# Performance work log

Hardware: AMD Instinct MI355X
Metric: run time of the kernel (lower is better)

The kernel has to match this reference:

```python
import jax, jax.numpy as jnp
import numpy as np

VOCAB, EMB = 30000, 300
HEADS, DPH = 8, 50
AD = HEADS * DPH            # att_dim_total = 400
MAX_LINES, MAX_WPL = 128, 32
BATCH = 16
NEG = 1e7                   # padding-mask penalty, matches torch source


def _split_heads(x):
    # [N, S, AD] -> [N, H, S, D]
    return x.reshape(x.shape[0], -1, HEADS, DPH).transpose(0, 2, 1, 3)


def _attention(q, k, v, mask_q=None, mask_k=None, mask_v=None):
    # Faithful port of MTHiSAN._attention. Note the (oddly named) torch masks:
    #   mask_q masks the KEY axis of scores, mask_k/mask_v zero the QUERY axis.
    scale = float(np.sqrt(q.shape[-1]))
    scores = jnp.einsum('bhqd,bhkd->bhqk', q, k) / scale
    if mask_q is not None:
        scores = scores - NEG * (~mask_q)[:, None, None, :].astype(scores.dtype)
    w = jax.nn.softmax(scores, axis=-1)
    if mask_k is not None:
        w = w * mask_k[:, None, :, None].astype(w.dtype)
    out = jnp.einsum('bhqk,bhkd->bhqd', w, v)
    if mask_v is not None:
        out = out * mask_v[:, None, :, None].astype(out.dtype)
    return out


def _forward(docs, emb, wq_w, wq_b, wk_w, wk_b, wv_w, wv_b, w_tgt,
             lq_w, lq_b, lk_w, lk_b, lv_w, lv_b, l_tgt,
             fc1_w, fc1_b, fc2_w, fc2_b):
    B = docs.shape[0]
    d = docs[:, :MAX_LINES * MAX_WPL].reshape(B * MAX_LINES, MAX_WPL)
    mask_w = d != 0                               # [B*L, W]
    mask_l = mask_w.sum(-1) != 0                  # [B*L]  non-empty lines
    # NOTE: instead of gathering non-empty lines (data-dependent shape), we keep
    # full shapes; masked word attention yields exact zeros for empty lines,
    # equivalent to the torch scatter into new_zeros.
    we = emb[d]                                   # [B*L, W, E] (dropout = eval/no-op)
    wq = jax.nn.elu(_split_heads(we @ wq_w + wq_b))
    wk = jax.nn.elu(_split_heads(we @ wk_w + wk_b))
    wv = jax.nn.elu(_split_heads(we @ wv_w + wv_b))
    watt = _attention(wq, wk, wv, mask_w, mask_w, mask_w)   # [B*L,H,W,D]
    # learned word-level target query (Linear(1, AD)(ones) == weight vector)
    tgt = jnp.broadcast_to(w_tgt.reshape(1, HEADS, 1, DPH),
                           (B * MAX_LINES, HEADS, 1, DPH))
    line_e = _attention(tgt, wk, watt, mask_q=mask_w)       # [B*L,H,1,D]
    line_e = line_e.transpose(0, 2, 1, 3).reshape(B * MAX_LINES, AD)
    line_e = line_e * mask_l[:, None].astype(line_e.dtype)  # zero empty lines
    line_e = line_e.reshape(B, MAX_LINES, AD)
    mask_l2 = mask_l.reshape(B, MAX_LINES)
    lq = jax.nn.elu(_split_heads(line_e @ lq_w + lq_b))
    lk = jax.nn.elu(_split_heads(line_e @ lk_w + lk_b))
    lv = jax.nn.elu(_split_heads(line_e @ lv_w + lv_b))
    latt = _attention(lq, lk, lv, mask_l2, mask_l2, mask_l2)  # [B,H,L,D]
    dtgt = jnp.broadcast_to(l_tgt.reshape(1, HEADS, 1, DPH), (B, HEADS, 1, DPH))
    doc_e = _attention(dtgt, lk, latt, mask_q=mask_l2)        # [B,H,1,D]
    doc_e = doc_e.transpose(0, 2, 1, 3).reshape(B, AD)
    logits1 = doc_e @ fc1_w + fc1_b   # task 'site'      [B,70]
    logits2 = doc_e @ fc2_w + fc2_b   # task 'histology' [B,512]
    return jnp.concatenate([logits1, logits2], axis=1)


def setup_inputs() -> dict:
    key = jax.random.key(0)
    ks = jax.random.split(key, 20)
    xavier = lambda k, i, o: (jax.random.normal(k, (i, o), jnp.float32)
                              * np.float32(np.sqrt(2.0 / (i + o))))
    emb = jax.random.normal(ks[0], (VOCAB, EMB), jnp.float32) * 0.02
    emb = emb.at[0].set(0.0)  # padding row zeroed as in __init__
    docs = jax.random.randint(ks[1], (BATCH, MAX_LINES * MAX_WPL), 0, VOCAB)
    z = lambda n: jnp.zeros((n,), jnp.float32)
    return dict(
        docs=docs, emb=emb,
        wq_w=xavier(ks[2], EMB, AD), wq_b=z(AD),
        wk_w=xavier(ks[3], EMB, AD), wk_b=z(AD),
        wv_w=xavier(ks[4], EMB, AD), wv_b=z(AD),
        w_tgt=jax.random.uniform(ks[5], (AD,), jnp.float32),
        lq_w=xavier(ks[6], AD, AD), lq_b=z(AD),
        lk_w=xavier(ks[7], AD, AD), lk_b=z(AD),
        lv_w=xavier(ks[8], AD, AD), lv_b=z(AD),
        l_tgt=jax.random.uniform(ks[9], (AD,), jnp.float32),
        fc1_w=xavier(ks[10], AD, 70), fc1_b=z(70),
        fc2_w=xavier(ks[11], AD, 512), fc2_b=z(512),
    )


def reference(docs, emb, wq_w, wq_b, wk_w, wk_b, wv_w, wv_b, w_tgt,
              lq_w, lq_b, lk_w, lk_b, lv_w, lv_b, l_tgt,
              fc1_w, fc1_b, fc2_w, fc2_b):
    return _forward(docs, emb, wq_w, wq_b, wk_w, wk_b, wv_w, wv_b, w_tgt,
                    lq_w, lq_b, lk_w, lk_b, lv_w, lv_b, l_tgt,
                    fc1_w, fc1_b, fc2_w, fc2_b)
```

## Files before the change

### kernel.cpp

```cpp
#include <hip/hip_runtime.h>
#include <math.h>

#define NLINES 2048
#define WPL 32
#define EMBD 300
#define AD 400
#define NH 8
#define DPH 50
#define QKV_S 52
#define SC_S 36
#define BATCH 16
#define LPD 128
#define NCOLS 1200
#define NPAD 1280
#define WLINE_FL 39936
#define HBLK 4992

typedef __bf16 bf16;
typedef bf16  v8bf  __attribute__((ext_vector_type(8)));
typedef float v4f   __attribute__((ext_vector_type(4)));
typedef float v16f  __attribute__((ext_vector_type(16)));

__device__ __forceinline__ float elu(float x) {
    return x > 0.f ? x : expm1f(x);
}
__device__ __forceinline__ float elu_fast(float x) {
    return x > 0.f ? x : (__expf(x) - 1.f);
}

#define SCALE 7.0710678118654755f

__global__ void split_rows_packed(const float* __restrict__ src,
                                  bf16* __restrict__ pk,
                                  int rows, int K, int K2)
{
    long idx = (long)blockIdx.x * 256 + threadIdx.x;
    if (idx >= (long)rows * K2) return;
    int r = (int)(idx / K2), k = (int)(idx - (long)r * K2);
    float x = (k < K) ? src[(long)r * K + k] : 0.f;
    bf16 h = (bf16)x;
    float hf = (float)h;
    bf16 l = (bf16)(x - hf);
    const long p = ((long)r * (K2 >> 3) + (k >> 3)) * 16 + (k & 7);
    pk[p] = h; pk[p + 8] = l;
}

__global__ void split_wt_packed(const float* __restrict__ W0, const float* __restrict__ W1,
                                const float* __restrict__ W2,
                                const float* __restrict__ B0, const float* __restrict__ B1,
                                const float* __restrict__ B2,
                                bf16* __restrict__ pk,
                                float* __restrict__ biasCat, int K, int K2)
{
    long idx = (long)blockIdx.x * 256 + threadIdx.x;
    if (idx >= (long)NPAD * K2) return;
    int n = (int)(idx / K2), k = (int)(idx - (long)n * K2);
    float x = 0.f;
    if (k < K && n < NCOLS) {
        int p = n / 400, c = n - p * 400;
        const float* W = (p == 0) ? W0 : (p == 1) ? W1 : W2;
        x = W[(long)k * 400 + c];
    }
    bf16 h = (bf16)x;
    float hf = (float)h;
    bf16 l = (bf16)(x - hf);
    const long pidx = ((long)(k >> 3) * NPAD + n) * 16 + (k & 7);
    pk[pidx] = h; pk[pidx + 8] = l;
    if (k == 0) {
        float b = 0.f;
        if (n < NCOLS) {
            int p = n / 400, c = n - p * 400;
            const float* Bp = (p == 0) ? B0 : (p == 1) ? B1 : B2;
            b = Bp[c];
        }
        biasCat[n] = b;
    }
}

__launch_bounds__(256, 4)
__global__ void mfma_gemm(const bf16* __restrict__ Ap,
                          const int* __restrict__ docs,
                          const bf16* __restrict__ Bp,
                          const float* __restrict__ biasCat,
                          float* __restrict__ C, int K2, int word_layout)
{
    __shared__ int tok[128];

    const int tid = threadIdx.x;

    const int total = (int)(gridDim.x * gridDim.y);
    int flat = (int)(blockIdx.y * gridDim.x + blockIdx.x);
    if ((total & 7) == 0) flat = (flat & 7) * (total >> 3) + (flat >> 3);
    const int bx = flat % (int)gridDim.x;
    const int by = flat / (int)gridDim.x;
    const int row0 = by * 128;
    const int n0 = bx * 128;

    if (tid < 128) tok[tid] = docs ? docs[row0 + tid] : (row0 + tid);
    __syncthreads();

    const int wv = tid >> 6, lane = tid & 63;
    const int half = lane >> 5, r32 = lane & 31;
    const int wm0 = (wv >> 1) * 64, wn0 = (wv & 1) * 64;

    const int colA = n0 + wn0 + r32;
    const int colB = colA + 32;

    const long a0 = (long)tok[wm0 + r32]      * ((long)K2 * 2);
    const long a1 = (long)tok[wm0 + 32 + r32] * ((long)K2 * 2);

    v16f acc[2][2];
    #pragma unroll
    for (int a = 0; a < 2; ++a)
        #pragma unroll
        for (int b = 0; b < 2; ++b) acc[a][b] = (v16f)0.f;

    const int nk = K2 >> 5;
    for (int kt = 0; kt < nk; ++kt) {
        #pragma unroll
        for (int ks = 0; ks < 2; ++ks) {
            const int k0 = kt * 32 + (ks * 2 + half) * 8;
            const bf16* bg = Bp + (long)(k0 >> 3) * NPAD * 16;
            const long ka = (long)k0 * 2;
            v8bf fb_h[2], fb_l[2], fa_h[2], fa_l[2];
            fb_h[0] = *(const v8bf*)&bg[(long)colA * 16];
            fb_l[0] = *(const v8bf*)&bg[(long)colA * 16 + 8];
            fb_h[1] = *(const v8bf*)&bg[(long)colB * 16];
            fb_l[1] = *(const v8bf*)&bg[(long)colB * 16 + 8];
            fa_h[0] = *(const v8bf*)&Ap[a0 + ka];
            fa_l[0] = *(const v8bf*)&Ap[a0 + ka + 8];
            fa_h[1] = *(const v8bf*)&Ap[a1 + ka];
            fa_l[1] = *(const v8bf*)&Ap[a1 + ka + 8];

            #pragma unroll
            for (int mt = 0; mt < 2; ++mt)
                #pragma unroll
                for (int nt = 0; nt < 2; ++nt)
                    acc[mt][nt] = __builtin_amdgcn_mfma_f32_32x32x16_bf16(fa_h[mt], fb_h[nt], acc[mt][nt], 0, 0, 0);
            #pragma unroll
            for (int mt = 0; mt < 2; ++mt)
                #pragma unroll
                for (int nt = 0; nt < 2; ++nt)
                    acc[mt][nt] = __builtin_amdgcn_mfma_f32_32x32x16_bf16(fa_h[mt], fb_l[nt], acc[mt][nt], 0, 0, 0);
            #pragma unroll
            for (int mt = 0; mt < 2; ++mt)
                #pragma unroll
                for (int nt = 0; nt < 2; ++nt)
                    acc[mt][nt] = __builtin_amdgcn_mfma_f32_32x32x16_bf16(fa_l[mt], fb_h[nt], acc[mt][nt], 0, 0, 0);
        }
    }

    if (word_layout) {
        #pragma unroll
        for (int nt = 0; nt < 2; ++nt) {
            const int col = n0 + wn0 + nt * 32 + r32;
            if (col >= NCOLS) continue;
            const float bv = biasCat[col];
            const int p = col / 400;
            const int rem = col - p * 400;
            const int hh = rem / 50;
            const int d  = rem - hh * 50;
            #pragma unroll
            for (int mt = 0; mt < 2; ++mt) {
                const int rbase = row0 + wm0 + mt * 32 + 4 * half;
                #pragma unroll
                for (int rg = 0; rg < 16; ++rg) {
                    const int row = rbase + (rg & 3) + 8 * (rg >> 2);
                    const int ln = row >> 5, r = row & 31;
                    const long base = (((long)ln * NH + hh) * 3 + p) * 1664 + r * 52;
                    const float x = acc[mt][nt][rg] + bv;
                    C[base + d] = elu_fast(x);
                    if (d == 49) {
                        float2 z; z.x = 0.f; z.y = 0.f;
                        *(float2*)&C[base + 50] = z;
                    }
                }
            }
        }
    } else {
        #pragma unroll
        for (int nt = 0; nt < 2; ++nt) {
            const int col = n0 + wn0 + nt * 32 + r32;
            if (col >= NCOLS) continue;
            const float bv = biasCat[col];
            #pragma unroll
            for (int mt = 0; mt < 2; ++mt) {
                const int rbase = row0 + wm0 + mt * 32 + 4 * half;
                #pragma unroll
                for (int rg = 0; rg < 16; ++rg) {
                    const int row = rbase + (rg & 3) + 8 * (rg >> 2);
                    const float x = acc[mt][nt][rg] + bv;
                    C[(long)row * NCOLS + col] = elu_fast(x);
                }
            }
        }
    }
}

__launch_bounds__(256)
__global__ void word_attn4(const float* __restrict__ qkvw, const int* __restrict__ docs,
                           const float* __restrict__ w_tgt,
                           float* __restrict__ line_e, float* __restrict__ mask_l)
{
    __shared__ __align__(16) float sh[HBLK];
    __shared__ float sc[32 * 33];
    __shared__ float msk[WPL];
    __shared__ float tw[WPL];
    __shared__ float coefA[WPL];
    __shared__ float part[8][33];
    __shared__ float cw[WPL];
    __shared__ float vpart[4][64];
    __shared__ float tg[52];
    __shared__ float mls_s;

    const int tid = threadIdx.x;
    const int line = blockIdx.x >> 3;
    const int h = blockIdx.x & 7;

    if (tid < WPL) msk[tid] = (docs[line * WPL + tid] != 0) ? 1.f : 0.f;
    if (tid >= 64 && tid < 116) tg[tid - 64] = (tid - 64 < DPH) ? w_tgt[h * DPH + tid - 64] : 0.f;

    const float* src = qkvw + ((long)line * NH + h) * HBLK;
    for (int i = tid; i < HBLK / 4; i += 256)
        *(float4*)&sh[i * 4] = *(const float4*)&src[i * 4];
    __syncthreads();

    if (tid == 0) {
        float m = 0.f;
        for (int w = 0; w < WPL; ++w) m = fmaxf(m, msk[w]);
        mls_s = m;
        if (h == 0) mask_l[line] = m;
    }

    const int j = tid >> 3, kg = tid & 7;
    float4 qv[13];
    #pragma unroll
    for (int i = 0; i < 13; ++i) qv[i] = *(const float4*)&sh[j * 52 + i * 4];

    float e4[4];
    float m = -1e30f;
    #pragma unroll
    for (int c = 0; c < 4; ++c) {
        const int kk = kg * 4 + c;
        const float* kr = &sh[1664 + kk * 52];
        float s = 0.f;
        #pragma unroll
        for (int i = 0; i < 13; ++i) {
            const float4 kv = *(const float4*)&kr[i * 4];
            s += qv[i].x * kv.x + qv[i].y * kv.y + qv[i].z * kv.z + qv[i].w * kv.w;
        }
        s = s / SCALE - 1e7f * (1.f - msk[kk]);
        e4[c] = s;
        m = fmaxf(m, s);
    }
    m = fmaxf(m, __shfl_xor(m, 1));
    m = fmaxf(m, __shfl_xor(m, 2));
    m = fmaxf(m, __shfl_xor(m, 4));
    float rsum = 0.f;
    #pragma unroll
    for (int c = 0; c < 4; ++c) { e4[c] = __expf(e4[c] - m); rsum += e4[c]; }
    rsum += __shfl_xor(rsum, 1);
    rsum += __shfl_xor(rsum, 2);
    rsum += __shfl_xor(rsum, 4);
    #pragma unroll
    for (int c = 0; c < 4; ++c) sc[j * 33 + kg * 4 + c] = e4[c];

    if (tid < WPL) {
        const float* kr = &sh[1664 + tid * 52];
        float s = 0.f;
        #pragma unroll
        for (int i = 0; i < 25; ++i)
            s += tg[2 * i] * kr[2 * i] + tg[2 * i + 1] * kr[2 * i + 1];
        s = s / SCALE - 1e7f * (1.f - msk[tid]);
        float tm = s;
        #pragma unroll
        for (int off = 16; off >= 1; off >>= 1) tm = fmaxf(tm, __shfl_xor(tm, off, 32));
        const float te = __expf(s - tm);
        float tsum = te;
        #pragma unroll
        for (int off = 16; off >= 1; off >>= 1) tsum += __shfl_xor(tsum, off, 32);
        tw[tid] = te / tsum;
    }
    __syncthreads();

    if (kg == 0) coefA[j] = tw[j] * msk[j] / rsum;
    __syncthreads();

    {
        const int k = tid & 31, jg = tid >> 5;
        float cv = 0.f;
        #pragma unroll
        for (int t = 0; t < 4; ++t) {
            const int jj = jg * 4 + t;
            cv += coefA[jj] * sc[jj * 33 + k];
        }
        part[jg][k] = cv;
    }
    __syncthreads();
    if (tid < WPL) {
        float cv = 0.f;
        #pragma unroll
        for (int g = 0; g < 8; ++g) cv += part[g][tid];
        cw[tid] = cv;
    }
    __syncthreads();

    {
        const int d = tid & 63, kh = tid >> 6;
        float acc = 0.f;
        if (d < 52) {
            #pragma unroll
            for (int t = 0; t < 8; ++t) {
                const int k = kh * 8 + t;
                acc += cw[k] * sh[3328 + k * 52 + d];
            }
        }
        vpart[kh][d] = acc;
    }
    __syncthreads();
    if (tid < DPH) {
        const float o = vpart[0][tid] + vpart[1][tid] + vpart[2][tid] + vpart[3][tid];
        line_e[(long)line * AD + h * DPH + tid] = o * mls_s;
    }
}

__launch_bounds__(256)
__global__ void line_attn2(const float* __restrict__ Q, const float* __restrict__ Kp,
                           const float* __restrict__ Vp,
                           long DS, long HS, long LS,
                           const float* __restrict__ l_tgt, const float* __restrict__ mask_l,
                           float* __restrict__ doc_e)
{
    __shared__ float kl[LPD * 52];
    __shared__ float sc[64 * 130];
    __shared__ float ml[LPD];
    __shared__ float tw[LPD];
    __shared__ float cw[LPD];
    __shared__ float coefA[64];
    __shared__ float pm[4 * 64];
    __shared__ float ps[4 * 64];
    __shared__ float tg[52];
    __shared__ float rr[2];
    __shared__ float vpart[2][64];

    const int tid = threadIdx.x;
    const int doc = blockIdx.x >> 3;
    const int h = blockIdx.x & 7;
    const float* qbase = Q + doc * DS + h * HS;
    const float* kbase = Kp + doc * DS + h * HS;
    const float* vbase = Vp + doc * DS + h * HS;

    if (tid < LPD) { ml[tid] = mask_l[doc * LPD + tid]; cw[tid] = 0.f; }
    if (tid < 52) tg[tid] = (tid < DPH) ? l_tgt[h * DPH + tid] : 0.f;
    for (int idx = tid; idx < LPD * 52; idx += 256) {
        const int r = idx / 52, d = idx - r * 52;
        kl[idx] = (d < DPH) ? kbase[(long)r * LS + d] : 0.f;
    }
    __syncthreads();

    if (tid < LPD) {
        const float* kr = &kl[tid * 52];
        float s = 0.f;
        #pragma unroll
        for (int i = 0; i < 25; ++i)
            s += tg[2 * i] * kr[2 * i] + tg[2 * i + 1] * kr[2 * i + 1];
        tw[tid] = s / SCALE - 1e7f * (1.f - ml[tid]);
    }
    __syncthreads();
    if (tid < 64) {
        float a = fmaxf(tw[tid], tw[64 + tid]);
        #pragma unroll
        for (int off = 32; off >= 1; off >>= 1) a = fmaxf(a, __shfl_xor(a, off));
        if (tid == 0) rr[0] = a;
    }
    __syncthreads();
    if (tid < 64) {
        const float tm2 = rr[0];
        float a = __expf(tw[tid] - tm2) + __expf(tw[64 + tid] - tm2);
        #pragma unroll
        for (int off = 32; off >= 1; off >>= 1) a += __shfl_xor(a, off);
        if (tid == 0) rr[1] = a;
    }
    __syncthreads();
    if (tid < LPD) tw[tid] = __expf(tw[tid] - rr[0]) / rr[1];
    __syncthreads();

    const int j2 = tid & 63;
    const int kq = tid >> 6;

    for (int g = 0; g < 2; ++g) {
        const int j = g * 64 + j2;
        float2 qv[25];
        #pragma unroll
        for (int i = 0; i < 25; ++i)
            qv[i] = *(const float2*)(qbase + (long)j * LS + 2 * i);

        float m = -1e30f;
        for (int c = 0; c < 32; ++c) {
            const int k = kq * 32 + c;
            const float* kr = &kl[k * 52];
            float s = 0.f;
            #pragma unroll
            for (int i = 0; i < 25; ++i)
                s += qv[i].x * kr[2 * i] + qv[i].y * kr[2 * i + 1];
            s = s / SCALE - 1e7f * (1.f - ml[k]);
            sc[j2 * 130 + k] = s;
            m = fmaxf(m, s);
        }
        pm[kq * 64 + j2] = m;
        __syncthreads();
        const float rowm = fmaxf(fmaxf(pm[j2], pm[64 + j2]),
                                 fmaxf(pm[128 + j2], pm[192 + j2]));
        float sum = 0.f;
        for (int c = 0; c < 32; ++c) {
            const int k = kq * 32 + c;
            const float e = __expf(sc[j2 * 130 + k] - rowm);
            sc[j2 * 130 + k] = e;
            sum += e;
        }
        ps[kq * 64 + j2] = sum;
        __syncthreads();
        if (kq == 0) {
            const float rs = ps[j2] + ps[64 + j2] + ps[128 + j2] + ps[192 + j2];
            coefA[j2] = tw[j] * ml[j] / rs;
        }
        __syncthreads();
        if (tid < LPD) {
            float cv = 0.f;
            for (int jj = 0; jj < 64; ++jj)
                cv += coefA[jj] * sc[jj * 130 + tid];
            cw[tid] += cv;
        }
        __syncthreads();
    }

    const int d = tid & 63;
    const int half = (tid >> 6) & 1;
    if (tid < 128 && d < DPH) {
        float acc = 0.f;
        for (int k = half * 64; k < half * 64 + 64; ++k)
            acc += cw[k] * vbase[(long)k * LS + d];
        vpart[half][d] = acc;
    }
    __syncthreads();
    if (tid < DPH)
        doc_e[doc * AD + h * DPH + tid] = vpart[0][tid] + vpart[1][tid];
}

__launch_bounds__(256)
__global__ void word_attn(const float* __restrict__ qkv, const int* __restrict__ docs,
                          const float* __restrict__ w_tgt,
                          float* __restrict__ line_e, float* __restrict__ mask_l)
{
    __shared__ float qs[WPL * QKV_S];
    __shared__ float ks[WPL * QKV_S];
    __shared__ float vs[WPL * QKV_S];
    __shared__ float sc[WPL * SC_S];
    __shared__ float ts[WPL], tw[WPL], cw[WPL], msk[WPL];
    __shared__ float mls;

    const int tid = threadIdx.x;
    const int line = blockIdx.x;

    if (tid < WPL) msk[tid] = (docs[line * WPL + tid] != 0) ? 1.f : 0.f;
    __syncthreads();
    if (tid == 0) {
        float ml = 0.f;
        for (int w = 0; w < WPL; ++w) ml = fmaxf(ml, msk[w]);
        mls = ml;
        mask_l[line] = ml;
    }
    for (int h = 0; h < NH; ++h) {
        for (int idx = tid; idx < WPL * DPH; idx += 256) {
            const int r = idx / DPH, d = idx - r * DPH;
            const size_t base = (size_t)(line * WPL + r) * NCOLS + h * DPH + d;
            qs[r * QKV_S + d] = qkv[base];
            ks[r * QKV_S + d] = qkv[base + 400];
            vs[r * QKV_S + d] = qkv[base + 800];
        }
        __syncthreads();
        {
            const int j = tid >> 3, kg = tid & 7;
            #pragma unroll
            for (int c = 0; c < 4; ++c) {
                const int kk = kg * 4 + c;
                float s = 0.f;
                for (int dd = 0; dd < DPH; ++dd)
                    s += qs[j * QKV_S + dd] * ks[kk * QKV_S + dd];
                sc[j * SC_S + kk] = s / SCALE - 1e7f * (1.f - msk[kk]);
            }
        }
        if (tid < WPL) {
            float s = 0.f;
            for (int dd = 0; dd < DPH; ++dd)
                s += w_tgt[h * DPH + dd] * ks[tid * QKV_S + dd];
            ts[tid] = s / SCALE - 1e7f * (1.f - msk[tid]);
        }
        __syncthreads();
        if (tid < WPL) {
            const int j = tid;
            float m = -1e30f;
            for (int kk = 0; kk < WPL; ++kk) m = fmaxf(m, sc[j * SC_S + kk]);
            float sum = 0.f;
            for (int kk = 0; kk < WPL; ++kk) {
                const float e = expf(sc[j * SC_S + kk] - m);
                sc[j * SC_S + kk] = e;
                sum += e;
            }
            const float inv = 1.f / sum;
            for (int kk = 0; kk < WPL; ++kk) sc[j * SC_S + kk] *= inv;
        } else if (tid == WPL) {
            float m = -1e30f;
            for (int jj = 0; jj < WPL; ++jj) m = fmaxf(m, ts[jj]);
            float sum = 0.f;
            for (int jj = 0; jj < WPL; ++jj) { const float e = expf(ts[jj] - m); tw[jj] = e; sum += e; }
            const float inv = 1.f / sum;
            for (int jj = 0; jj < WPL; ++jj) tw[jj] *= inv;
        }
        __syncthreads();
        if (tid < WPL) {
            const int kk = tid;
            float c = 0.f;
            for (int jj = 0; jj < WPL; ++jj) c += tw[jj] * msk[jj] * sc[jj * SC_S + kk];
            cw[kk] = c;
        }
        __syncthreads();
        if (tid < DPH) {
            float acc = 0.f;
            for (int kk = 0; kk < WPL; ++kk) acc += cw[kk] * vs[kk * QKV_S + tid];
            line_e[line * AD + h * DPH + tid] = acc * mls;
        }
        __syncthreads();
    }
}

__launch_bounds__(256, 2)
__global__ void gemm_qkv(const float* __restrict__ Asrc,
                         const int* __restrict__ docs,
                         const float* __restrict__ emb,
                         const float* __restrict__ W0, const float* __restrict__ W1,
                         const float* __restrict__ W2,
                         const float* __restrict__ B0, const float* __restrict__ B1,
                         const float* __restrict__ B2,
                         float* __restrict__ C, int M, int K)
{
    __shared__ __align__(16) float As[32][132];
    __shared__ __align__(16) float Bs[32][132];

    const int tid = threadIdx.x;
    const int row0 = blockIdx.x * 128;
    const int n0 = blockIdx.y * 128;
    const int tc = tid & 15, tr = tid >> 4;

    float acc[2][2][4][4];
    #pragma unroll
    for (int a = 0; a < 2; ++a)
        #pragma unroll
        for (int b = 0; b < 2; ++b)
            #pragma unroll
            for (int c = 0; c < 4; ++c)
                #pragma unroll
                for (int d = 0; d < 4; ++d) acc[a][b][c][d] = 0.f;

    const int ma = tid & 127;
    const int kq = tid >> 7;
    const float* arow;
    if (docs) arow = emb + (size_t)docs[row0 + ma] * EMBD;
    else      arow = Asrc + (size_t)(row0 + ma) * K;

    const int gcol = n0 + ma;
    const int p = gcol / 400;
    const int ccol = gcol - p * 400;
    const float* Wp = (p == 0) ? W0 : (p == 1) ? W1 : W2;
    const bool colv = gcol < NCOLS;

    const int nk = (K + 31) >> 5;
    for (int ck = 0; ck < nk; ++ck) {
        const int k0 = ck * 32;
        #pragma unroll
        for (int f = 0; f < 4; ++f) {
            const int kl = kq * 16 + f * 4;
            const int kg = k0 + kl;
            float4 v = make_float4(0.f, 0.f, 0.f, 0.f);
            if (kg < K) v = *(const float4*)(arow + kg);
            As[kl + 0][ma] = v.x;
            As[kl + 1][ma] = v.y;
            As[kl + 2][ma] = v.z;
            As[kl + 3][ma] = v.w;
        }
        #pragma unroll
        for (int i = 0; i < 16; ++i) {
            const int kl = kq * 16 + i;
            const int kg = k0 + kl;
            float v = 0.f;
            if (colv && kg < K) v = Wp[(size_t)kg * 400 + ccol];
            Bs[kl][ma] = v;
        }
        __syncthreads();

        #pragma unroll 8
        for (int k = 0; k < 32; ++k) {
            const float4 a0 = *(const float4*)&As[k][tr * 4];
            const float4 a1 = *(const float4*)&As[k][64 + tr * 4];
            const float4 b0 = *(const float4*)&Bs[k][tc * 4];
            const float4 b1 = *(const float4*)&Bs[k][64 + tc * 4];
            const float ar[2][4] = {{a0.x, a0.y, a0.z, a0.w}, {a1.x, a1.y, a1.z, a1.w}};
            const float br[2][4] = {{b0.x, b0.y, b0.z, b0.w}, {b1.x, b1.y, b1.z, b1.w}};
            #pragma unroll
            for (int im = 0; im < 2; ++im)
                #pragma unroll
                for (int in_ = 0; in_ < 2; ++in_)
                    #pragma unroll
                    for (int rr = 0; rr < 4; ++rr)
                        #pragma unroll
                        for (int cc = 0; cc < 4; ++cc)
                            acc[im][in_][rr][cc] += ar[im][rr] * br[in_][cc];
        }
        __syncthreads();
    }

    #pragma unroll
    for (int in_ = 0; in_ < 2; ++in_) {
        const int ncol = n0 + in_ * 64 + tc * 4;
        if (ncol >= NCOLS) continue;
        const int pj = ncol / 400;
        const int cj = ncol - pj * 400;
        const float* Bp = (pj == 0) ? B0 : (pj == 1) ? B1 : B2;
        const float4 bv = *(const float4*)(Bp + cj);
        #pragma unroll
        for (int im = 0; im < 2; ++im) {
            #pragma unroll
            for (int rr = 0; rr < 4; ++rr) {
                const int row = row0 + im * 64 + tr * 4 + rr;
                float4 o;
                o.x = elu(acc[im][in_][rr][0] + bv.x);
                o.y = elu(acc[im][in_][rr][1] + bv.y);
                o.z = elu(acc[im][in_][rr][2] + bv.z);
                o.w = elu(acc[im][in_][rr][3] + bv.w);
                *(float4*)(C + (size_t)row * NCOLS + ncol) = o;
            }
        }
    }
}

__global__ void logits_kernel(const float* __restrict__ doc_e,
                              const float* __restrict__ fc1_w, const float* __restrict__ fc1_b,
                              const float* __restrict__ fc2_w, const float* __restrict__ fc2_b,
                              float* __restrict__ out)
{
    int o = blockIdx.x * blockDim.x + threadIdx.x;
    if (o >= BATCH * 582) return;
    int b = o / 582, jj = o - b * 582;
    const float* de = doc_e + b * AD;
    float acc;
    if (jj < 70) {
        acc = fc1_b[jj];
        for (int k = 0; k < AD; ++k) acc += de[k] * fc1_w[k * 70 + jj];
    } else {
        int j2 = jj - 70;
        acc = fc2_b[j2];
        for (int k = 0; k < AD; ++k) acc += de[k] * fc2_w[k * 512 + j2];
    }
    out[o] = acc;
}

extern "C" void kernel_launch(void* const* d_in, const int* in_sizes, int n_in,
                              void* d_out, int out_size, void* d_ws, size_t ws_size,
                              hipStream_t stream) {
    const int*   docs  = (const int*)  d_in[0];
    const float* emb   = (const float*)d_in[1];
    const float* wq_w  = (const float*)d_in[2];
    const float* wq_b  = (const float*)d_in[3];
    const float* wk_w  = (const float*)d_in[4];
    const float* wk_b  = (const float*)d_in[5];
    const float* wv_w  = (const float*)d_in[6];
    const float* wv_b  = (const float*)d_in[7];
    const float* w_tgt = (const float*)d_in[8];
    const float* lq_w  = (const float*)d_in[9];
    const float* lq_b  = (const float*)d_in[10];
    const float* lk_w  = (const float*)d_in[11];
    const float* lk_b  = (const float*)d_in[12];
    const float* lv_w  = (const float*)d_in[13];
    const float* lv_b  = (const float*)d_in[14];
    const float* l_tgt = (const float*)d_in[15];
    const float* fc1_w = (const float*)d_in[16];
    const float* fc1_b = (const float*)d_in[17];
    const float* fc2_w = (const float*)d_in[18];
    const float* fc2_b = (const float*)d_in[19];
    float* out = (float*)d_out;
    float* ws = (float*)d_ws;

    const long O_LINE_E = 0;
    const long O_MASK_L = 819200;
    const long O_DOC_E  = 821248;
    const long O_BIAS_W = 827648;
    const long O_BIAS_L = 828928;
    const long O_EMB_H  = 830208;
    const long O_WTW_H  = 10430208;
    const long O_WTL_H  = 10839808;
    const long O_LE_H   = 11372288;
    const long O_R      = 12224256;

    const long LINE_QKV_FL = (long)NLINES * NCOLS;
    long ws_fl = (long)(ws_size / 4);
    long Rcap = ws_fl - O_R;

    if (Rcap >= LINE_QKV_FL) {
        float* line_e = ws + O_LINE_E;
        float* mask_l = ws + O_MASK_L;
        float* doc_e  = ws + O_DOC_E;
        float* bias_w = ws + O_BIAS_W;
        float* bias_l = ws + O_BIAS_L;
        bf16* embp = (bf16*)(ws + O_EMB_H);
        bf16* wtwp = (bf16*)(ws + O_WTW_H);
        bf16* wtlp = (bf16*)(ws + O_WTL_H);
        bf16* lep  = (bf16*)(ws + O_LE_H);
        float* R   = ws + O_R;

        split_rows_packed<<<(30000L * 320 + 255) / 256, 256, 0, stream>>>(emb, embp, 30000, 300, 320);
        split_wt_packed<<<((long)NPAD * 320 + 255) / 256, 256, 0, stream>>>(wq_w, wk_w, wv_w,
                                                                            wq_b, wk_b, wv_b,
                                                                            wtwp, bias_w, 300, 320);
        split_wt_packed<<<((long)NPAD * 416 + 255) / 256, 256, 0, stream>>>(lq_w, lk_w, lv_w,
                                                                            lq_b, lk_b, lv_b,
                                                                            wtlp, bias_l, 400, 416);

        long maxl = Rcap / WLINE_FL;
        if (maxl > 1024) maxl = 1024;
        long chunk = (maxl / 4) * 4;
        if (chunk < 4) chunk = 4;
        for (long c0 = 0; c0 < NLINES; c0 += chunk) {
            long cl = NLINES - c0 < chunk ? NLINES - c0 : chunk;
            dim3 g1(10, (unsigned)((cl * 32) / 128));
            mfma_gemm<<<g1, 256, 0, stream>>>(embp, docs + c0 * WPL,
                                              wtwp, bias_w, R, 320, 1);
            word_attn4<<<(unsigned)(cl * NH), 256, 0, stream>>>(R, docs + c0 * WPL, w_tgt,
                                                                line_e + c0 * AD, mask_l + c0);
        }

        split_rows_packed<<<((long)NLINES * 416 + 255) / 256, 256, 0, stream>>>(line_e, lep,
                                                                                NLINES, 400, 416);
        dim3 g2(10, NLINES / 128);
        mfma_gemm<<<g2, 256, 0, stream>>>(lep, nullptr, wtlp, bias_l, R, 416, 0);
        line_attn2<<<BATCH * NH, 256, 0, stream>>>(R, R + 400, R + 800,
                                                   (long)LPD * NCOLS, (long)DPH, (long)NCOLS,
                                                   l_tgt, mask_l, doc_e);
        logits_kernel<<<(BATCH * 582 + 255) / 256, 256, 0, stream>>>(doc_e, fc1_w, fc1_b,
                                                                     fc2_w, fc2_b, out);
    } else {
        const long F_FIXED = 827648;
        const long PER_LINE_FL = (long)WPL * NCOLS;
        float* line_e = ws;
        float* mask_l = ws + 819200;
        float* doc_e  = ws + 821248;
        float* R      = ws + F_FIXED;
        long Rcap2 = ws_fl - F_FIXED;

        long maxl = Rcap2 / PER_LINE_FL;
        if (maxl > NLINES) maxl = NLINES;
        long maxl4 = (maxl / 4) * 4;
        int nc = (int)((NLINES + maxl4 - 1) / maxl4);
        int chunk = (int)((NLINES + nc - 1) / nc);
        chunk = ((chunk + 3) / 4) * 4;

        for (int c0 = 0; c0 < NLINES; c0 += chunk) {
            int cl = NLINES - c0 < chunk ? NLINES - c0 : chunk;
            dim3 g1((cl * 32) / 128, 10);
            gemm_qkv<<<g1, 256, 0, stream>>>(nullptr, docs + (size_t)c0 * WPL, emb,
                                             wq_w, wk_w, wv_w, wq_b, wk_b, wv_b,
                                             R, cl * 32, EMBD);
            word_attn<<<cl, 256, 0, stream>>>(R, docs + (size_t)c0 * WPL, w_tgt,
                                              line_e + (size_t)c0 * AD, mask_l + c0);
        }
        dim3 g2(16, 10);
        gemm_qkv<<<g2, 256, 0, stream>>>(line_e, nullptr, emb,
                                         lq_w, lk_w, lv_w, lq_b, lk_b, lv_b,
                                         R, NLINES, AD);
        line_attn2<<<BATCH * NH, 256, 0, stream>>>(R, R + 400, R + 800,
                                                   (long)LPD * NCOLS, (long)DPH, (long)NCOLS,
                                                   l_tgt, mask_l, doc_e);
        logits_kernel<<<(BATCH * 582 + 255) / 256, 256, 0, stream>>>(doc_e, fc1_w, fc1_b,
                                                                     fc2_w, fc2_b, out);
    }
}
```

Baseline: 652.5 us.

## Fuse word-level QKV GEMM and word attention into one per-line kernel

Replaces the chunked word-level MFMA GEMM plus separate word_attn4 kernel with a single fused_word kernel, one 512-thread block per line. The block gathers embedding rows into LDS, computes the Q/K/V projection for four heads per phase with split-bf16 MFMAs, applies ELU into shared memory, and runs the attention directly without writing the large QKV intermediate to global memory. This removes the global round trip of the intermediate and the chunk loop, in exchange for lower occupancy (launch bounds 512,1), B-operand loads read directly from global per block with less reuse across lines, and the GEMM being split into two head phases.

```diff
diff --git a/kernel.cpp b/kernel.cpp
--- a/kernel.cpp
+++ b/kernel.cpp
@@ -13,12 +13,10 @@
 #define LPD 128
 #define NCOLS 1200
 #define NPAD 1280
-#define WLINE_FL 39936
 #define HBLK 4992
 
 typedef __bf16 bf16;
 typedef bf16  v8bf  __attribute__((ext_vector_type(8)));
-typedef float v4f   __attribute__((ext_vector_type(4)));
 typedef float v16f  __attribute__((ext_vector_type(16)));
 
 __device__ __forceinline__ float elu(float x) {
@@ -77,6 +75,220 @@
     }
 }
 
+__launch_bounds__(512, 1)
+__global__ void fused_word(const bf16* __restrict__ Ap,
+                           const int* __restrict__ docs,
+                           const bf16* __restrict__ Bp,
+                           const float* __restrict__ biasCat,
+                           const float* __restrict__ w_tgt,
+                           float* __restrict__ line_e, float* __restrict__ mask_l)
+{
+    __shared__ __align__(16) bf16 Alds[40 * 2 * 32 * 8];
+    __shared__ __align__(16) float qkv[3][4][32][52];
+    __shared__ float sc2[2][32 * 33];
+    __shared__ float tw2[2][WPL];
+    __shared__ float coefA2[2][WPL];
+    __shared__ float part2[2][8][33];
+    __shared__ float cw2[2][WPL];
+    __shared__ float vpart2[2][4][64];
+    __shared__ float tg2[2][52];
+    __shared__ float msk[WPL];
+    __shared__ float mls_s;
+
+    const int tid = threadIdx.x;
+    const int line = blockIdx.x;
+
+    if (tid < WPL) msk[tid] = (docs[line * WPL + tid] != 0) ? 1.f : 0.f;
+    __syncthreads();
+    if (tid == 0) {
+        float m = 0.f;
+        for (int w = 0; w < WPL; ++w) m = fmaxf(m, msk[w]);
+        mls_s = m;
+        mask_l[line] = m;
+    }
+
+    for (int slot = tid; slot < 40 * 2 * 32; slot += 512) {
+        const int row = slot & 31;
+        const int hl  = (slot >> 5) & 1;
+        const int kf  = slot >> 6;
+        const int token = docs[line * WPL + row];
+        *(v8bf*)&Alds[slot * 8] = *(const v8bf*)&Ap[((long)token * 40 + kf) * 16 + hl * 8];
+    }
+
+    const int wv = tid >> 6;
+    const int lane = tid & 63;
+    const int half = lane >> 5, r32 = lane & 31;
+    const int sub = tid >> 8;
+    const int t2  = tid & 255;
+
+    for (int ph = 0; ph < 2; ++ph) {
+        const int h0 = ph * 4;
+
+        for (int i = tid; i < 3 * 4 * 32 * 52; i += 512)
+            ((float*)qkv)[i] = 0.f;
+        __syncthreads();
+
+        {
+            const int ta = wv;
+            const int tb = wv + 8;
+            const bool has3 = (wv + 16) < 21;
+            const int tc = has3 ? wv + 16 : tb;
+            const int c0a = (ta / 7) * 400 + (ph * 6 + ta % 7) * 32;
+            const int c0b = (tb / 7) * 400 + (ph * 6 + tb % 7) * 32;
+            const int c0c = (tc / 7) * 400 + (ph * 6 + tc % 7) * 32;
+
+            v16f a0 = (v16f)0.f, a1 = (v16f)0.f, a2 = (v16f)0.f;
+            #pragma unroll 4
+            for (int s = 0; s < 20; ++s) {
+                const int kf = 2 * s + half;
+                const v8bf fah = *(const v8bf*)&Alds[((kf * 2 + 0) * 32 + r32) * 8];
+                const v8bf fal = *(const v8bf*)&Alds[((kf * 2 + 1) * 32 + r32) * 8];
+                const bf16* bg = Bp + (long)kf * NPAD * 16;
+                const v8bf fbh0 = *(const v8bf*)&bg[(c0a + r32) * 16];
+                const v8bf fbl0 = *(const v8bf*)&bg[(c0a + r32) * 16 + 8];
+                const v8bf fbh1 = *(const v8bf*)&bg[(c0b + r32) * 16];
+                const v8bf fbl1 = *(const v8bf*)&bg[(c0b + r32) * 16 + 8];
+                const v8bf fbh2 = *(const v8bf*)&bg[(c0c + r32) * 16];
+                const v8bf fbl2 = *(const v8bf*)&bg[(c0c + r32) * 16 + 8];
+                a0 = __builtin_amdgcn_mfma_f32_32x32x16_bf16(fah, fbh0, a0, 0, 0, 0);
+                a1 = __builtin_amdgcn_mfma_f32_32x32x16_bf16(fah, fbh1, a1, 0, 0, 0);
+                a2 = __builtin_amdgcn_mfma_f32_32x32x16_bf16(fah, fbh2, a2, 0, 0, 0);
+                a0 = __builtin_amdgcn_mfma_f32_32x32x16_bf16(fah, fbl0, a0, 0, 0, 0);
+                a1 = __builtin_amdgcn_mfma_f32_32x32x16_bf16(fah, fbl1, a1, 0, 0, 0);
+                a2 = __builtin_amdgcn_mfma_f32_32x32x16_bf16(fah, fbl2, a2, 0, 0, 0);
+                a0 = __builtin_amdgcn_mfma_f32_32x32x16_bf16(fal, fbh0, a0, 0, 0, 0);
+                a1 = __builtin_amdgcn_mfma_f32_32x32x16_bf16(fal, fbh1, a1, 0, 0, 0);
+                a2 = __builtin_amdgcn_mfma_f32_32x32x16_bf16(fal, fbh2, a2, 0, 0, 0);
+            }
+
+            const v16f* accs[3] = { &a0, &a1, &a2 };
+            const int   c0s[3]  = { c0a, c0b, c0c };
+            #pragma unroll
+            for (int u = 0; u < 3; ++u) {
+                const int col = c0s[u] + r32;
+                const int p = col / 400;
+                const int rem = col - p * 400;
+                const int hh = rem / 50;
+                if (rem < 400 && hh >= h0 && hh < h0 + 4) {
+                    const int d = rem - hh * 50;
+                    const float bv = biasCat[col];
+                    const v16f& a = *accs[u];
+                    #pragma unroll
+                    for (int rg = 0; rg < 16; ++rg) {
+                        const int row = (rg & 3) + 8 * (rg >> 2) + 4 * half;
+                        qkv[p][hh - h0][row][d] = elu_fast(a[rg] + bv);
+                    }
+                }
+            }
+        }
+        __syncthreads();
+
+        for (int hp = 0; hp < 2; ++hp) {
+            const int hl = hp * 2 + sub;
+            const int h  = h0 + hl;
+            const float* q  = &qkv[0][hl][0][0];
+            const float* kk_ = &qkv[1][hl][0][0];
+            const float* vv_ = &qkv[2][hl][0][0];
+
+            if (t2 < 52) tg2[sub][t2] = (t2 < DPH) ? w_tgt[h * DPH + t2] : 0.f;
+            __syncthreads();
+
+            const int j = t2 >> 3, kg = t2 & 7;
+            float4 qv[13];
+            #pragma unroll
+            for (int i = 0; i < 13; ++i) qv[i] = *(const float4*)&q[j * 52 + i * 4];
+
+            float e4[4];
+            float m = -1e30f;
+            #pragma unroll
+            for (int c = 0; c < 4; ++c) {
+                const int kk = kg * 4 + c;
+                const float* kr = &kk_[kk * 52];
+                float s = 0.f;
+                #pragma unroll
+                for (int i = 0; i < 13; ++i) {
+                    const float4 kv = *(const float4*)&kr[i * 4];
+                    s += qv[i].x * kv.x + qv[i].y * kv.y + qv[i].z * kv.z + qv[i].w * kv.w;
+                }
+                s = s / SCALE - 1e7f * (1.f - msk[kk]);
+                e4[c] = s;
+                m = fmaxf(m, s);
+            }
+            m = fmaxf(m, __shfl_xor(m, 1));
+            m = fmaxf(m, __shfl_xor(m, 2));
+            m = fmaxf(m, __shfl_xor(m, 4));
+            float rsum = 0.f;
+            #pragma unroll
+            for (int c = 0; c < 4; ++c) { e4[c] = __expf(e4[c] - m); rsum += e4[c]; }
+            rsum += __shfl_xor(rsum, 1);
+            rsum += __shfl_xor(rsum, 2);
+            rsum += __shfl_xor(rsum, 4);
+            #pragma unroll
+            for (int c = 0; c < 4; ++c) sc2[sub][j * 33 + kg * 4 + c] = e4[c];
+
+            if (t2 < WPL) {
+                const float* kr = &kk_[t2 * 52];
+                float s = 0.f;
+                #pragma unroll
+                for (int i = 0; i < 25; ++i)
+                    s += tg2[sub][2 * i] * kr[2 * i] + tg2[sub][2 * i + 1] * kr[2 * i + 1];
+                s = s / SCALE - 1e7f * (1.f - msk[t2]);
+                float tm = s;
+                #pragma unroll
+                for (int off = 16; off >= 1; off >>= 1) tm = fmaxf(tm, __shfl_xor(tm, off, 32));
+                const float te = __expf(s - tm);
+                float tsum = te;
+                #pragma unroll
+                for (int off = 16; off >= 1; off >>= 1) tsum += __shfl_xor(tsum, off, 32);
+                tw2[sub][t2] = te / tsum;
+            }
+            __syncthreads();
+
+            if (kg == 0) coefA2[sub][j] = tw2[sub][j] * msk[j] / rsum;
+            __syncthreads();
+
+            {
+                const int k = t2 & 31, jg = t2 >> 5;
+                float cv = 0.f;
+                #pragma unroll
+                for (int t = 0; t < 4; ++t) {
+                    const int jj = jg * 4 + t;
+                    cv += coefA2[sub][jj] * sc2[sub][jj * 33 + k];
+                }
+                part2[sub][jg][k] = cv;
+            }
+            __syncthreads();
+            if (t2 < WPL) {
+                float cv = 0.f;
+                #pragma unroll
+                for (int g = 0; g < 8; ++g) cv += part2[sub][g][t2];
+                cw2[sub][t2] = cv;
+            }
+            __syncthreads();
+
+            {
+                const int d = t2 & 63, kh = t2 >> 6;
+                float acc = 0.f;
+                if (d < 52) {
+                    #pragma unroll
+                    for (int t = 0; t < 8; ++t) {
+                        const int k = kh * 8 + t;
+                        acc += cw2[sub][k] * vv_[k * 52 + d];
+                    }
+                }
+                vpart2[sub][kh][d] = acc;
+            }
+            __syncthreads();
+            if (t2 < DPH) {
+                const float o = vpart2[sub][0][t2] + vpart2[sub][1][t2]
+                              + vpart2[sub][2][t2] + vpart2[sub][3][t2];
+                line_e[(long)line * AD + h * DPH + t2] = o * mls_s;
+            }
+            __syncthreads();
+        }
+    }
+}
+
 __launch_bounds__(256, 4)
 __global__ void mfma_gemm(const bf16* __restrict__ Ap,
                           const int* __restrict__ docs,
@@ -194,133 +406,6 @@
                 }
             }
         }
-    }
-}
-
-__launch_bounds__(256)
-__global__ void word_attn4(const float* __restrict__ qkvw, const int* __restrict__ docs,
-                           const float* __restrict__ w_tgt,
-                           float* __restrict__ line_e, float* __restrict__ mask_l)
-{
-    __shared__ __align__(16) float sh[HBLK];
-    __shared__ float sc[32 * 33];
-    __shared__ float msk[WPL];
-    __shared__ float tw[WPL];
-    __shared__ float coefA[WPL];
-    __shared__ float part[8][33];
-    __shared__ float cw[WPL];
-    __shared__ float vpart[4][64];
-    __shared__ float tg[52];
-    __shared__ float mls_s;
-
-    const int tid = threadIdx.x;
-    const int line = blockIdx.x >> 3;
-    const int h = blockIdx.x & 7;
-
-    if (tid < WPL) msk[tid] = (docs[line * WPL + tid] != 0) ? 1.f : 0.f;
-    if (tid >= 64 && tid < 116) tg[tid - 64] = (tid - 64 < DPH) ? w_tgt[h * DPH + tid - 64] : 0.f;
-
-    const float* src = qkvw + ((long)line * NH + h) * HBLK;
-    for (int i = tid; i < HBLK / 4; i += 256)
-        *(float4*)&sh[i * 4] = *(const float4*)&src[i * 4];
-    __syncthreads();
-
-    if (tid == 0) {
-        float m = 0.f;
-        for (int w = 0; w < WPL; ++w) m = fmaxf(m, msk[w]);
-        mls_s = m;
-        if (h == 0) mask_l[line] = m;
-    }
-
-    const int j = tid >> 3, kg = tid & 7;
-    float4 qv[13];
-    #pragma unroll
-    for (int i = 0; i < 13; ++i) qv[i] = *(const float4*)&sh[j * 52 + i * 4];
-
-    float e4[4];
-    float m = -1e30f;
-    #pragma unroll
-    for (int c = 0; c < 4; ++c) {
-        const int kk = kg * 4 + c;
-        const float* kr = &sh[1664 + kk * 52];
-        float s = 0.f;
-        #pragma unroll
-        for (int i = 0; i < 13; ++i) {
-            const float4 kv = *(const float4*)&kr[i * 4];
-            s += qv[i].x * kv.x + qv[i].y * kv.y + qv[i].z * kv.z + qv[i].w * kv.w;
-        }
-        s = s / SCALE - 1e7f * (1.f - msk[kk]);
-        e4[c] = s;
-        m = fmaxf(m, s);
-    }
-    m = fmaxf(m, __shfl_xor(m, 1));
-    m = fmaxf(m, __shfl_xor(m, 2));
-    m = fmaxf(m, __shfl_xor(m, 4));
-    float rsum = 0.f;
-    #pragma unroll
-    for (int c = 0; c < 4; ++c) { e4[c] = __expf(e4[c] - m); rsum += e4[c]; }
-    rsum += __shfl_xor(rsum, 1);
-    rsum += __shfl_xor(rsum, 2);
-    rsum += __shfl_xor(rsum, 4);
-    #pragma unroll
-    for (int c = 0; c < 4; ++c) sc[j * 33 + kg * 4 + c] = e4[c];
-
-    if (tid < WPL) {
-        const float* kr = &sh[1664 + tid * 52];
-        float s = 0.f;
-        #pragma unroll
-        for (int i = 0; i < 25; ++i)
-            s += tg[2 * i] * kr[2 * i] + tg[2 * i + 1] * kr[2 * i + 1];
-        s = s / SCALE - 1e7f * (1.f - msk[tid]);
-        float tm = s;
-        #pragma unroll
-        for (int off = 16; off >= 1; off >>= 1) tm = fmaxf(tm, __shfl_xor(tm, off, 32));
-        const float te = __expf(s - tm);
-        float tsum = te;
-        #pragma unroll
-        for (int off = 16; off >= 1; off >>= 1) tsum += __shfl_xor(tsum, off, 32);
-        tw[tid] = te / tsum;
-    }
-    __syncthreads();
-
-    if (kg == 0) coefA[j] = tw[j] * msk[j] / rsum;
-    __syncthreads();
-
-    {
-        const int k = tid & 31, jg = tid >> 5;
-        float cv = 0.f;
-        #pragma unroll
-        for (int t = 0; t < 4; ++t) {
-            const int jj = jg * 4 + t;
-            cv += coefA[jj] * sc[jj * 33 + k];
-        }
-        part[jg][k] = cv;
-    }
-    __syncthreads();
-    if (tid < WPL) {
-        float cv = 0.f;
-        #pragma unroll
-        for (int g = 0; g < 8; ++g) cv += part[g][tid];
-        cw[tid] = cv;
-    }
-    __syncthreads();
-
-    {
-        const int d = tid & 63, kh = tid >> 6;
-        float acc = 0.f;
-        if (d < 52) {
-            #pragma unroll
-            for (int t = 0; t < 8; ++t) {
-                const int k = kh * 8 + t;
-                acc += cw[k] * sh[3328 + k * 52 + d];
-            }
-        }
-        vpart[kh][d] = acc;
-    }
-    __syncthreads();
-    if (tid < DPH) {
-        const float o = vpart[0][tid] + vpart[1][tid] + vpart[2][tid] + vpart[3][tid];
-        line_e[(long)line * AD + h * DPH + tid] = o * mls_s;
     }
 }
 
@@ -725,18 +810,8 @@
                                                                             lq_b, lk_b, lv_b,
                                                                             wtlp, bias_l, 400, 416);
 
-        long maxl = Rcap / WLINE_FL;
-        if (maxl > 1024) maxl = 1024;
-        long chunk = (maxl / 4) * 4;
-        if (chunk < 4) chunk = 4;
-        for (long c0 = 0; c0 < NLINES; c0 += chunk) {
-            long cl = NLINES - c0 < chunk ? NLINES - c0 : chunk;
-            dim3 g1(10, (unsigned)((cl * 32) / 128));
-            mfma_gemm<<<g1, 256, 0, stream>>>(embp, docs + c0 * WPL,
-                                              wtwp, bias_w, R, 320, 1);
-            word_attn4<<<(unsigned)(cl * NH), 256, 0, stream>>>(R, docs + c0 * WPL, w_tgt,
-                                                                line_e + c0 * AD, mask_l + c0);
-        }
+        fused_word<<<NLINES, 512, 0, stream>>>(embp, docs, wtwp, bias_w, w_tgt,
+                                               line_e, mask_l);
 
         split_rows_packed<<<((long)NLINES * 416 + 255) / 256, 256, 0, stream>>>(line_e, lep,
                                                                                 NLINES, 400, 416);
```

New measurement: 561.1 us. 1.16x faster.

## Fuse word-level QKV projection GEMM with word attention per line

Applied to the files above, without the earlier changes.

Replaces the separate word-level MFMA GEMM plus word_attn4 kernel pair, which ran in chunks through a global QKV buffer, with one fused kernel per line. Each 512-thread block gathers the embedding rows for its 32 tokens into LDS once, computes Q/K/V for each head with MFMA into shared memory, and runs the masked attention and target pooling in place. This removes the large intermediate global write and read and the chunked launches. In exchange, each block streams the whole weight matrix from global or L2 per line with a small 32-row M tile, and the heads are processed serially with many barriers, so weight reuse and occupancy are lower.

```diff
diff --git a/kernel.cpp b/kernel.cpp
--- a/kernel.cpp
+++ b/kernel.cpp
@@ -13,12 +13,11 @@
 #define LPD 128
 #define NCOLS 1200
 #define NPAD 1280
-#define WLINE_FL 39936
 #define HBLK 4992
+#define QP 54
 
 typedef __bf16 bf16;
 typedef bf16  v8bf  __attribute__((ext_vector_type(8)));
-typedef float v4f   __attribute__((ext_vector_type(4)));
 typedef float v16f  __attribute__((ext_vector_type(16)));
 
 __device__ __forceinline__ float elu(float x) {
@@ -77,6 +76,186 @@
     }
 }
 
+__launch_bounds__(512, 2)
+__global__ void fused_word(const bf16* __restrict__ Ap,
+                           const int* __restrict__ docs,
+                           const bf16* __restrict__ Bp,
+                           const float* __restrict__ biasCat,
+                           const float* __restrict__ w_tgt,
+                           float* __restrict__ line_e, float* __restrict__ mask_l)
+{
+    __shared__ __align__(16) bf16 Alds[40 * 2 * 32 * 8];
+    __shared__ __align__(16) float qkv[3][32][QP];
+    __shared__ float sc[32 * 33];
+    __shared__ float part[16][33];
+    __shared__ float vpart[8][64];
+    __shared__ float tw[WPL];
+    __shared__ float coefA[WPL];
+    __shared__ float cw[WPL];
+    __shared__ float tg[52];
+    __shared__ float msk[WPL];
+    __shared__ float mls_s;
+
+    const int tid = threadIdx.x;
+    const int line = blockIdx.x;
+
+    if (tid < WPL) msk[tid] = (docs[line * WPL + tid] != 0) ? 1.f : 0.f;
+    __syncthreads();
+    if (tid == 0) {
+        float m = 0.f;
+        for (int w = 0; w < WPL; ++w) m = fmaxf(m, msk[w]);
+        mls_s = m;
+        mask_l[line] = m;
+    }
+
+    for (int slot = tid; slot < 40 * 2 * 32; slot += 512) {
+        const int row = slot & 31;
+        const int hl  = (slot >> 5) & 1;
+        const int kf  = slot >> 6;
+        const int token = docs[line * WPL + row];
+        *(v8bf*)&Alds[slot * 8] = *(const v8bf*)&Ap[((long)token * 40 + kf) * 16 + hl * 8];
+    }
+    __syncthreads();
+
+    const int wv = tid >> 6;
+    const int lane = tid & 63;
+    const int half = lane >> 5, r32 = lane & 31;
+
+    for (int h = 0; h < NH; ++h) {
+        if (wv < 6) {
+            const int proj = wv >> 1;
+            const int c0 = proj * 400 + h * 50 + (wv & 1) * 32;
+            v16f acc = (v16f)0.f;
+            #pragma unroll 4
+            for (int s = 0; s < 20; ++s) {
+                const int kf = 2 * s + half;
+                const v8bf fah = *(const v8bf*)&Alds[((kf * 2 + 0) * 32 + r32) * 8];
+                const v8bf fal = *(const v8bf*)&Alds[((kf * 2 + 1) * 32 + r32) * 8];
+                const bf16* bg = Bp + ((long)kf * NPAD + c0 + r32) * 16;
+                const v8bf fbh = *(const v8bf*)&bg[0];
+                const v8bf fbl = *(const v8bf*)&bg[8];
+                acc = __builtin_amdgcn_mfma_f32_32x32x16_bf16(fah, fbh, acc, 0, 0, 0);
+                acc = __builtin_amdgcn_mfma_f32_32x32x16_bf16(fah, fbl, acc, 0, 0, 0);
+                acc = __builtin_amdgcn_mfma_f32_32x32x16_bf16(fal, fbh, acc, 0, 0, 0);
+            }
+            const int d = (wv & 1) * 32 + r32;
+            if (d < DPH) {
+                const float bv = biasCat[c0 + r32];
+                #pragma unroll
+                for (int rg = 0; rg < 16; ++rg) {
+                    const int row = (rg & 3) + 8 * (rg >> 2) + 4 * half;
+                    qkv[proj][row][d] = elu_fast(acc[rg] + bv);
+                }
+            }
+        } else {
+            const int t = tid - 384;
+            if (t < 96) {
+                const int p = t / 32, row = t & 31;
+                qkv[p][row][50] = 0.f; qkv[p][row][51] = 0.f;
+                qkv[p][row][52] = 0.f; qkv[p][row][53] = 0.f;
+            } else if (t >= 96 && t < 148) {
+                const int i = t - 96;
+                tg[i] = (i < DPH) ? w_tgt[h * DPH + i] : 0.f;
+            }
+        }
+        __syncthreads();
+
+        const float* q   = &qkv[0][0][0];
+        const float* kk_ = &qkv[1][0][0];
+        const float* vv_ = &qkv[2][0][0];
+
+        const int j = tid >> 4, kg = tid & 15;
+        float2 qv[27];
+        #pragma unroll
+        for (int i = 0; i < 27; ++i) qv[i] = *(const float2*)&q[j * QP + 2 * i];
+
+        float e2[2];
+        float m = -1e30f;
+        #pragma unroll
+        for (int c = 0; c < 2; ++c) {
+            const int kk = kg * 2 + c;
+            const float* kr = &kk_[kk * QP];
+            float s = 0.f;
+            #pragma unroll
+            for (int i = 0; i < 27; ++i)
+                s += qv[i].x * kr[2 * i] + qv[i].y * kr[2 * i + 1];
+            s = s / SCALE - 1e7f * (1.f - msk[kk]);
+            e2[c] = s;
+            m = fmaxf(m, s);
+        }
+        m = fmaxf(m, __shfl_xor(m, 1, 16));
+        m = fmaxf(m, __shfl_xor(m, 2, 16));
+        m = fmaxf(m, __shfl_xor(m, 4, 16));
+        m = fmaxf(m, __shfl_xor(m, 8, 16));
+        float rsum = 0.f;
+        #pragma unroll
+        for (int c = 0; c < 2; ++c) { e2[c] = __expf(e2[c] - m); rsum += e2[c]; }
+        rsum += __shfl_xor(rsum, 1, 16);
+        rsum += __shfl_xor(rsum, 2, 16);
+        rsum += __shfl_xor(rsum, 4, 16);
+        rsum += __shfl_xor(rsum, 8, 16);
+        sc[j * 33 + kg * 2]     = e2[0];
+        sc[j * 33 + kg * 2 + 1] = e2[1];
+
+        if (tid < WPL) {
+            const float* kr = &kk_[tid * QP];
+            float s = 0.f;
+            #pragma unroll
+            for (int i = 0; i < 25; ++i)
+                s += tg[2 * i] * kr[2 * i] + tg[2 * i + 1] * kr[2 * i + 1];
+            s = s / SCALE - 1e7f * (1.f - msk[tid]);
+            float tm = s;
+            #pragma unroll
+            for (int off = 16; off >= 1; off >>= 1) tm = fmaxf(tm, __shfl_xor(tm, off, 32));
+            const float te = __expf(s - tm);
+            float tsum = te;
+            #pragma unroll
+            for (int off = 16; off >= 1; off >>= 1) tsum += __shfl_xor(tsum, off, 32);
+            tw[tid] = te / tsum;
+        }
+        __syncthreads();
+
+        if (kg == 0) coefA[j] = tw[j] * msk[j] / rsum;
+        __syncthreads();
+
+        {
+            const int k = tid & 31, jg = tid >> 5;
+            const int j0 = jg * 2;
+            part[jg][k] = coefA[j0] * sc[j0 * 33 + k]
+                        + coefA[j0 + 1] * sc[(j0 + 1) * 33 + k];
+        }
+        __syncthreads();
+        if (tid < WPL) {
+            float cv = 0.f;
+            #pragma unroll
+            for (int g = 0; g < 16; ++g) cv += part[g][tid];
+            cw[tid] = cv;
+        }
+        __syncthreads();
+
+        {
+            const int d = tid & 63, kh = tid >> 6;
+            float acc = 0.f;
+            if (d < QP) {
+                #pragma unroll
+                for (int t = 0; t < 4; ++t) {
+                    const int k = kh * 4 + t;
+                    acc += cw[k] * vv_[k * QP + d];
+                }
+            }
+            vpart[kh][d] = acc;
+        }
+        __syncthreads();
+        if (tid < DPH) {
+            float o = 0.f;
+            #pragma unroll
+            for (int g = 0; g < 8; ++g) o += vpart[g][tid];
+            line_e[(long)line * AD + h * DPH + tid] = o * mls_s;
+        }
+        __syncthreads();
+    }
+}
+
 __launch_bounds__(256, 4)
 __global__ void mfma_gemm(const bf16* __restrict__ Ap,
                           const int* __restrict__ docs,
@@ -194,133 +373,6 @@
                 }
             }
         }
-    }
-}
-
-__launch_bounds__(256)
-__global__ void word_attn4(const float* __restrict__ qkvw, const int* __restrict__ docs,
-                           const float* __restrict__ w_tgt,
-                           float* __restrict__ line_e, float* __restrict__ mask_l)
-{
-    __shared__ __align__(16) float sh[HBLK];
-    __shared__ float sc[32 * 33];
-    __shared__ float msk[WPL];
-    __shared__ float tw[WPL];
-    __shared__ float coefA[WPL];
-    __shared__ float part[8][33];
-    __shared__ float cw[WPL];
-    __shared__ float vpart[4][64];
-    __shared__ float tg[52];
-    __shared__ float mls_s;
-
-    const int tid = threadIdx.x;
-    const int line = blockIdx.x >> 3;
-    const int h = blockIdx.x & 7;
-
-    if (tid < WPL) msk[tid] = (docs[line * WPL + tid] != 0) ? 1.f : 0.f;
-    if (tid >= 64 && tid < 116) tg[tid - 64] = (tid - 64 < DPH) ? w_tgt[h * DPH + tid - 64] : 0.f;
-
-    const float* src = qkvw + ((long)line * NH + h) * HBLK;
-    for (int i = tid; i < HBLK / 4; i += 256)
-        *(float4*)&sh[i * 4] = *(const float4*)&src[i * 4];
-    __syncthreads();
-
-    if (tid == 0) {
-        float m = 0.f;
-        for (int w = 0; w < WPL; ++w) m = fmaxf(m, msk[w]);
-        mls_s = m;
-        if (h == 0) mask_l[line] = m;
-    }
-
-    const int j = tid >> 3, kg = tid & 7;
-    float4 qv[13];
-    #pragma unroll
-    for (int i = 0; i < 13; ++i) qv[i] = *(const float4*)&sh[j * 52 + i * 4];
-
-    float e4[4];
-    float m = -1e30f;
-    #pragma unroll
-    for (int c = 0; c < 4; ++c) {
-        const int kk = kg * 4 + c;
-        const float* kr = &sh[1664 + kk * 52];
-        float s = 0.f;
-        #pragma unroll
-        for (int i = 0; i < 13; ++i) {
-            const float4 kv = *(const float4*)&kr[i * 4];
-            s += qv[i].x * kv.x + qv[i].y * kv.y + qv[i].z * kv.z + qv[i].w * kv.w;
-        }
-        s = s / SCALE - 1e7f * (1.f - msk[kk]);
-        e4[c] = s;
-        m = fmaxf(m, s);
-    }
-    m = fmaxf(m, __shfl_xor(m, 1));
-    m = fmaxf(m, __shfl_xor(m, 2));
-    m = fmaxf(m, __shfl_xor(m, 4));
-    float rsum = 0.f;
-    #pragma unroll
-    for (int c = 0; c < 4; ++c) { e4[c] = __expf(e4[c] - m); rsum += e4[c]; }
-    rsum += __shfl_xor(rsum, 1);
-    rsum += __shfl_xor(rsum, 2);
-    rsum += __shfl_xor(rsum, 4);
-    #pragma unroll
-    for (int c = 0; c < 4; ++c) sc[j * 33 + kg * 4 + c] = e4[c];
-
-    if (tid < WPL) {
-        const float* kr = &sh[1664 + tid * 52];
-        float s = 0.f;
-        #pragma unroll
-        for (int i = 0; i < 25; ++i)
-            s += tg[2 * i] * kr[2 * i] + tg[2 * i + 1] * kr[2 * i + 1];
-        s = s / SCALE - 1e7f * (1.f - msk[tid]);
-        float tm = s;
-        #pragma unroll
-        for (int off = 16; off >= 1; off >>= 1) tm = fmaxf(tm, __shfl_xor(tm, off, 32));
-        const float te = __expf(s - tm);
-        float tsum = te;
-        #pragma unroll
-        for (int off = 16; off >= 1; off >>= 1) tsum += __shfl_xor(tsum, off, 32);
-        tw[tid] = te / tsum;
-    }
-    __syncthreads();
-
-    if (kg == 0) coefA[j] = tw[j] * msk[j] / rsum;
-    __syncthreads();
-
-    {
-        const int k = tid & 31, jg = tid >> 5;
-        float cv = 0.f;
-        #pragma unroll
-        for (int t = 0; t < 4; ++t) {
-            const int jj = jg * 4 + t;
-            cv += coefA[jj] * sc[jj * 33 + k];
-        }
-        part[jg][k] = cv;
-    }
-    __syncthreads();
-    if (tid < WPL) {
-        float cv = 0.f;
-        #pragma unroll
-        for (int g = 0; g < 8; ++g) cv += part[g][tid];
-        cw[tid] = cv;
-    }
-    __syncthreads();
-
-    {
-        const int d = tid & 63, kh = tid >> 6;
-        float acc = 0.f;
-        if (d < 52) {
-            #pragma unroll
-            for (int t = 0; t < 8; ++t) {
-                const int k = kh * 8 + t;
-                acc += cw[k] * sh[3328 + k * 52 + d];
-            }
-        }
-        vpart[kh][d] = acc;
-    }
-    __syncthreads();
-    if (tid < DPH) {
-        const float o = vpart[0][tid] + vpart[1][tid] + vpart[2][tid] + vpart[3][tid];
-        line_e[(long)line * AD + h * DPH + tid] = o * mls_s;
     }
 }
 
@@ -725,18 +777,8 @@
                                                                             lq_b, lk_b, lv_b,
                                                                             wtlp, bias_l, 400, 416);
 
-        long maxl = Rcap / WLINE_FL;
-        if (maxl > 1024) maxl = 1024;
-        long chunk = (maxl / 4) * 4;
-        if (chunk < 4) chunk = 4;
-        for (long c0 = 0; c0 < NLINES; c0 += chunk) {
-            long cl = NLINES - c0 < chunk ? NLINES - c0 : chunk;
-            dim3 g1(10, (unsigned)((cl * 32) / 128));
-            mfma_gemm<<<g1, 256, 0, stream>>>(embp, docs + c0 * WPL,
-                                              wtwp, bias_w, R, 320, 1);
-            word_attn4<<<(unsigned)(cl * NH), 256, 0, stream>>>(R, docs + c0 * WPL, w_tgt,
-                                                                line_e + c0 * AD, mask_l + c0);
-        }
+        fused_word<<<NLINES, 512, 0, stream>>>(embp, docs, wtwp, bias_w, w_tgt,
+                                               line_e, mask_l);
 
         split_rows_packed<<<((long)NLINES * 416 + 255) / 256, 256, 0, stream>>>(line_e, lep,
                                                                                 NLINES, 400, 416);
```

New measurement: 597.7 us. 1.09x faster.
